# Optimization experiments

Measured on AMD Instinct MI355X. Metric: run time of the kernel, lower is better.

The kernel has to match this reference:

```python
import jax, jax.numpy as jnp
import numpy as np

B, L, D, H, HD, FF, NL = 2, 2048, 1024, 16, 64, 4096, 2
EPS = 1e-5
NEG = -1e30


def setup_inputs() -> dict:
    key = jax.random.key(0)
    ks = jax.random.split(key, 20)
    x = jax.random.normal(ks[0], (B, L, D), jnp.float32)
    # RoPE tables, rotate-half convention: [L, HD]
    pos = jnp.arange(L, dtype=jnp.float32)
    freqs = 1.0 / (10000.0 ** (jnp.arange(0, HD, 2, dtype=jnp.float32) / HD))
    ang = pos[:, None] * freqs[None, :]              # [L, HD/2]
    cos = jnp.concatenate([jnp.cos(ang), jnp.cos(ang)], -1)
    sin = jnp.concatenate([jnp.sin(ang), jnp.sin(ang)], -1)
    s = 0.02
    wq = jax.random.normal(ks[1], (NL, D, D), jnp.float32) * s
    wk = jax.random.normal(ks[2], (NL, D, D), jnp.float32) * s
    wv = jax.random.normal(ks[3], (NL, D, D), jnp.float32) * s
    wo = jax.random.normal(ks[4], (NL, D, D), jnp.float32) * s
    w1 = jax.random.normal(ks[5], (NL, D, FF), jnp.float32) * s
    w2 = jax.random.normal(ks[6], (NL, FF, D), jnp.float32) * s
    w3 = jax.random.normal(ks[7], (NL, D, FF), jnp.float32) * s
    attn_norm = jnp.ones((NL, D), jnp.float32)
    mlp_norm = jnp.ones((NL, D), jnp.float32)
    final_norm = jnp.ones((D,), jnp.float32)
    rw1 = jax.random.normal(ks[8], (D, D), jnp.float32) * s
    rb1 = jnp.zeros((D,), jnp.float32)
    rw2 = jax.random.normal(ks[9], (D, 1), jnp.float32) * s
    rb2 = jnp.zeros((1,), jnp.float32)
    return dict(x=x, cos=cos, sin=sin, wq=wq, wk=wk, wv=wv, wo=wo,
                w1=w1, w2=w2, w3=w3, attn_norm=attn_norm, mlp_norm=mlp_norm,
                final_norm=final_norm, rw1=rw1, rb1=rb1, rw2=rw2, rb2=rb2)


def _rms(x, w):
    return x * jax.lax.rsqrt(jnp.mean(x * x, -1, keepdims=True) + EPS) * w


def _rope(t, cos, sin):
    # t: [B, L, H, HD]; cos/sin: [L, HD]
    t1, t2 = jnp.split(t, 2, axis=-1)
    rot = jnp.concatenate([-t2, t1], -1)
    return t * cos[None, :, None, :] + rot * sin[None, :, None, :]


def reference(x, cos, sin, wq, wk, wv, wo, w1, w2, w3,
              attn_norm, mlp_norm, final_norm, rw1, rb1, rw2, rb2):
    causal = jnp.tril(jnp.ones((L, L), bool))
    h = x
    for i in range(NL):  # small fixed layer loop
        a = _rms(h, attn_norm[i])
        q = _rope((a @ wq[i]).reshape(B, L, H, HD), cos, sin)
        k = _rope((a @ wk[i]).reshape(B, L, H, HD), cos, sin)
        v = (a @ wv[i]).reshape(B, L, H, HD)
        sc = jnp.einsum('bqhd,bkhd->bhqk', q, k) / np.float32(np.sqrt(HD))
        sc = jnp.where(causal, sc, NEG)
        o = jnp.einsum('bhqk,bkhd->bqhd', jax.nn.softmax(sc, -1), v)
        h = h + o.reshape(B, L, D) @ wo[i]
        m = _rms(h, mlp_norm[i])
        h = h + (jax.nn.silu(m @ w1[i]) * (m @ w3[i])) @ w2[i]
    h = _rms(h, final_norm)

    # router chunking: straight-through hard boundaries
    logits = (jax.nn.silu(h @ rw1 + rb1) @ rw2 + rb2)[..., 0]   # [B, L]
    probs = jax.nn.sigmoid(logits)
    hard = (probs > 0.5).astype(h.dtype)
    mask = probs + jax.lax.stop_gradient(hard - probs)
    mask = mask.at[:, 0].set(1.0)
    mhard = jax.lax.stop_gradient(mask)
    # select matrix: S padded to static upper bound L (rows >= counts are zero)
    cums = jnp.cumsum(mhard, -1)                                # [B, L]
    seg = jnp.arange(1, L + 1, dtype=cums.dtype)[None, :, None] # [1, S, 1]
    assignment = (cums[:, None, :] == seg).astype(h.dtype)      # [B, S, L]
    select = assignment * mask[:, None, :]
    compressed = jnp.einsum('bsl,bld->bsd', select, h)          # [B, S, D]
    boundary_positions = jnp.argsort(-mhard, axis=-1)           # stable in jax
    counts = mhard.sum(-1).astype(jnp.int32)
    avg_chunk_size = jnp.float32(L) / jnp.mean(counts.astype(jnp.float32))
    return (h, compressed, boundary_positions, counts, avg_chunk_size)
```

## Files before the change

### kernel.cpp

```cpp
#include <hip/hip_runtime.h>
#include <cmath>

#define B_  2
#define L_  2048
#define D_  1024
#define H_  16
#define FF_ 4096
#define NL_ 2
#define NT_ (B_*L_)
#define ND_ (NT_*D_)

typedef __attribute__((ext_vector_type(8))) short bf16x8;
typedef __attribute__((ext_vector_type(4))) float f32x4;

__device__ __forceinline__ short f2bf(float x){
  unsigned u = __builtin_bit_cast(unsigned, x);
  unsigned r = (u + 0x7fffu + ((u>>16)&1u)) >> 16;
  return (short)r;
}
__device__ __forceinline__ float bf2f(short s){
  unsigned u = ((unsigned)(unsigned short)s) << 16;
  return __builtin_bit_cast(float, u);
}
#define MFMA16(a,b,c) __builtin_amdgcn_mfma_f32_16x16x32_bf16(a,b,c,0,0,0)

__device__ __forceinline__ void gload16(const short* g, short* l){
  __builtin_amdgcn_global_load_lds((const __attribute__((address_space(1))) void*)g,
                                   (__attribute__((address_space(3))) void*)l, 16, 0, 0);
}

__device__ __forceinline__ int2 xcd_swizzle(){
  int gx = gridDim.x;
  int n  = gx * gridDim.y;
  int hw = blockIdx.x + gx*blockIdx.y;
  int logical = (hw&7)*(n>>3) + (hw>>3);
  return make_int2(logical % gx, logical / gx);
}

template<bool WF32>
__global__ __launch_bounds__(256) void k_rmsnorm_s(const float* __restrict__ in,
                                                   const float* __restrict__ w,
                                                   short* __restrict__ oh,
                                                   short* __restrict__ ol,
                                                   float* __restrict__ of){
  int row = blockIdx.x; int tid = threadIdx.x;
  float4 xv = ((const float4*)(in + (size_t)row*D_))[tid];
  float ss = xv.x*xv.x + xv.y*xv.y + xv.z*xv.z + xv.w*xv.w;
  #pragma unroll
  for (int off=32; off; off>>=1) ss += __shfl_xor(ss, off);
  __shared__ float wsum[4];
  if ((tid&63)==0) wsum[tid>>6] = ss;
  __syncthreads();
  float tot = wsum[0]+wsum[1]+wsum[2]+wsum[3];
  float scale = 1.0f / sqrtf(tot*(1.0f/(float)D_) + 1e-5f);
  float4 w4 = ((const float4*)w)[tid];
  float v[4] = {xv.x*scale*w4.x, xv.y*scale*w4.y, xv.z*scale*w4.z, xv.w*scale*w4.w};
  short4 hh, ll;
  short h0=f2bf(v[0]); hh.x=h0; ll.x=f2bf(v[0]-bf2f(h0));
  short h1=f2bf(v[1]); hh.y=h1; ll.y=f2bf(v[1]-bf2f(h1));
  short h2=f2bf(v[2]); hh.z=h2; ll.z=f2bf(v[2]-bf2f(h2));
  short h3=f2bf(v[3]); hh.w=h3; ll.w=f2bf(v[3]-bf2f(h3));
  *(short4*)(oh + (size_t)row*D_ + tid*4) = hh;
  *(short4*)(ol + (size_t)row*D_ + tid*4) = ll;
  if (WF32){
    float4 ov; ov.x=v[0]; ov.y=v[1]; ov.z=v[2]; ov.w=v[3];
    ((float4*)(of + (size_t)row*D_))[tid] = ov;
  }
}

__device__ __forceinline__ void wsplit_body(float (*t)[68], const float* __restrict__ src,
                                            short* __restrict__ dh, short* __restrict__ dl,
                                            int srcN, int kOff, int nOff, int KT,
                                            int bx, int by){
  int k0 = bx*64, n0v = by*64;
  int tid = threadIdx.x;
  #pragma unroll
  for (int p=0;p<4;p++){
    int r = p*16 + (tid>>4);
    int c4 = (tid&15)*4;
    float4 v = *(const float4*)(src + (size_t)(kOff + k0 + r)*srcN + nOff + n0v + c4);
    *(float4*)&t[r][c4] = v;
  }
  __syncthreads();
  int n = tid>>2, kk = (tid&3)*16;
  bf16x8 H0, L0, H1, L1;
  #pragma unroll
  for (int q=0;q<8;q++){
    float v = t[kk+q][n]; short h=f2bf(v); H0[q]=h; L0[q]=f2bf(v-bf2f(h));
  }
  #pragma unroll
  for (int q=0;q<8;q++){
    float v = t[kk+8+q][n]; short h=f2bf(v); H1[q]=h; L1[q]=f2bf(v-bf2f(h));
  }
  size_t dof = (size_t)(n0v + n)*KT + k0 + kk;
  *(bf16x8*)(dh + dof) = H0;  *(bf16x8*)(dh + dof + 8) = H1;
  *(bf16x8*)(dl + dof) = L0;  *(bf16x8*)(dl + dof + 8) = L1;
}

__global__ __launch_bounds__(256) void k_wsplit(const float* __restrict__ src,
                                                short* __restrict__ dh,
                                                short* __restrict__ dl,
                                                int srcN, int kOff, int nOff, int KT){
  __shared__ float t[64][68];
  wsplit_body(t, src, dh, dl, srcN, kOff, nOff, KT, blockIdx.x, blockIdx.y);
}

__global__ __launch_bounds__(256) void k_wsplit_qkv(const float* __restrict__ wq,
                                                    const float* __restrict__ wk,
                                                    const float* __restrict__ wv,
                                                    short* __restrict__ dh,
                                                    short* __restrict__ dl){
  __shared__ float t[64][68];
  int z = blockIdx.z;
  const float* s = (z==0)?wq:(z==1)?wk:wv;
  wsplit_body(t, s, dh + (size_t)z*1048576, dl + (size_t)z*1048576,
              1024, 0, 0, 1024, blockIdx.x, blockIdx.y);
}

__global__ __launch_bounds__(256) void k_wsplit_ffn(const float* __restrict__ w1,
                                                    const float* __restrict__ w3,
                                                    const float* __restrict__ w2,
                                                    short* __restrict__ w1h, short* __restrict__ w1l,
                                                    short* __restrict__ w3h, short* __restrict__ w3l,
                                                    short* __restrict__ w2h, short* __restrict__ w2l,
                                                    int hc){
  __shared__ float t[64][68];
  int z = blockIdx.z;
  if (z < 2){
    if (blockIdx.x >= 16) return;
    const float* s = z ? w3 : w1;
    wsplit_body(t, s, z?w3h:w1h, z?w3l:w1l, 4096, 0, hc*2048, 1024, blockIdx.x, blockIdx.y);
  } else {
    if (blockIdx.y >= 16) return;
    wsplit_body(t, w2, w2h, w2l, 1024, hc*2048, 0, 2048, blockIdx.x, blockIdx.y);
  }
}

__global__ __launch_bounds__(256,3) void k_qkv_mm(const short* __restrict__ Ah,
                                                  const short* __restrict__ Al,
                                                  const short* __restrict__ Wh,
                                                  const short* __restrict__ Wl,
                                                  short* __restrict__ OutH,
                                                  short* __restrict__ Vf){
  __shared__ short lds[32768];
  int tid = threadIdx.x, wid = tid>>6, lane = tid&63;
  int l15 = lane&15, l4 = lane>>4;
  int wr = wid>>1, wc = wid&1;
  int2 bxy = xcd_swizzle();
  int m0 = bxy.y*128, n0 = bxy.x*128;
  const int K = 1024;
  f32x4 acc[4][4];
  #pragma unroll
  for (int i=0;i<4;i++){
    #pragma unroll
    for (int j=0;j<4;j++) acc[i][j] = (f32x4){0.f,0.f,0.f,0.f};
  }
  const short* gsrc = (wid==0)?Ah:(wid==1)?Al:(wid==2)?Wh:Wl;
  int rb = (wid<2)? m0 : n0;
  int gcol = ((lane&7)^(lane>>3))*8;
  short* ldsw = lds + wid*8192;
  const short* gp0 = gsrc + (size_t)(rb + (lane>>3))*K + gcol;
  for (int k0=0; k0<K; k0+=64){
    const short* gp = gp0 + k0;
    #pragma unroll
    for (int lc=0; lc<16; ++lc)
      gload16(gp + (size_t)lc*8*K, ldsw + lc*512);
    __syncthreads();
    #pragma unroll
    for (int ks=0; ks<2; ++ks){
      bf16x8 af[4], alf[4], wf[4], wlf[4];
      int gs = ((ks*4 + l4) ^ (lane&7))*8;
      #pragma unroll
      for (int f=0; f<4; ++f){
        int ar = (wr*64 + f*16 + l15)*64 + gs;
        af[f]  = *(const bf16x8*)&lds[ar];
        alf[f] = *(const bf16x8*)&lds[8192 + ar];
        int wr2 = (wc*64 + f*16 + l15)*64 + gs;
        wf[f]  = *(const bf16x8*)&lds[16384 + wr2];
        wlf[f] = *(const bf16x8*)&lds[24576 + wr2];
      }
      __builtin_amdgcn_s_setprio(1);
      #pragma unroll
      for (int i=0;i<4;i++){
        #pragma unroll
        for (int j=0;j<4;j++){
          acc[i][j] = MFMA16(af[i],  wf[j],  acc[i][j]);
          acc[i][j] = MFMA16(alf[i], wf[j],  acc[i][j]);
          acc[i][j] = MFMA16(af[i],  wlf[j], acc[i][j]);
        }
      }
      __builtin_amdgcn_s_setprio(0);
    }
    __syncthreads();
  }
  int sel = n0 >> 10;
  int cb = (n0 & 1023) + wc*64;
  if (sel < 2){
    short* oh = OutH + (size_t)sel*8388608;
    short* ol = oh + 4194304;
    #pragma unroll
    for (int i=0;i<4;i++){
      #pragma unroll
      for (int j=0;j<4;j++){
        #pragma unroll
        for (int r=0;r<4;r++){
          size_t mg = (size_t)(m0 + wr*64 + i*16 + l4*4 + r);
          int ng = cb + j*16 + l15;
          float v = acc[i][j][r];
          short h = f2bf(v);
          oh[mg*1024 + ng] = h;
          ol[mg*1024 + ng] = f2bf(v - bf2f(h));
        }
      }
    }
  } else {
    #pragma unroll
    for (int i=0;i<4;i++){
      #pragma unroll
      for (int j=0;j<4;j++){
        #pragma unroll
        for (int r=0;r<4;r++){
          int mg = m0 + wr*64 + i*16 + l4*4 + r;
          int ng = cb + j*16 + l15;
          float v = acc[i][j][r];
          short hh2 = f2bf(v);
          short ll2 = f2bf(v - bf2f(hh2));
          int bb = mg >> 11, tt = mg & 2047;
          int hd = ng >> 6, kc = tt >> 5;
          int l4v = (tt>>3)&3, iv = tt&7;
          int dtv = (ng>>4)&3, l15v = ng&15;
          size_t base = ((size_t)((bb*16+hd)*64 + kc)*8 + dtv*2)*512 + (l4v*16+l15v)*8 + iv;
          Vf[base] = hh2;
          Vf[base + 512] = ll2;
        }
      }
    }
  }
}

template<int EPI>
__global__ __launch_bounds__(256,(EPI==3)?3:4) void k_mm64(const short* __restrict__ Ah,
                                                const short* __restrict__ Al,
                                                const short* __restrict__ Wh,
                                                const short* __restrict__ Wl,
                                                const short* __restrict__ W3h,
                                                const short* __restrict__ W3l,
                                                int K,
                                                float* __restrict__ Cf,
                                                const float* __restrict__ bias,
                                                short* __restrict__ Gh,
                                                short* __restrict__ Gl,
                                                int ldc){
  __shared__ short lds[(EPI==3)?32768:24576];
  int tid = threadIdx.x, wid = tid>>6, lane = tid&63;
  int l15 = lane&15, l4 = lane>>4;
  int2 bxy = xcd_swizzle();
  int m0 = bxy.y*128, n0 = bxy.x*64;
  f32x4 a1[2][4], a3[2][4];
  #pragma unroll
  for (int i=0;i<2;i++){
    #pragma unroll
    for (int j=0;j<4;j++){ a1[i][j]=(f32x4){0.f,0.f,0.f,0.f}; a3[i][j]=(f32x4){0.f,0.f,0.f,0.f}; }
  }
  int gcol = ((lane&7)^(lane>>3))*8;
  int l8 = lane>>3;
  const int NCH = (EPI==3)? 16 : 12;
  for (int k0=0; k0<K; k0+=64){
    for (int t=0; t<NCH; ++t){
      int c = wid*NCH + t;
      const short* sb; int row0; short* db;
      if (c < 32){
        sb = (c<16)? Ah : Al; row0 = m0 + (c&15)*8;
        db = lds + ((c<16)?0:8192) + (c&15)*512;
      } else {
        int wseg = (c-32)>>3;
        sb = (wseg==0)?Wh:(wseg==1)?Wl:(wseg==2)?W3h:W3l;
        row0 = n0 + (c&7)*8;
        db = lds + 16384 + wseg*4096 + (c&7)*512;
      }
      gload16(sb + (size_t)(row0 + l8)*K + k0 + gcol, db);
    }
    __syncthreads();
    #pragma unroll
    for (int ks=0; ks<2; ++ks){
      int gs = ((ks*4 + l4) ^ (lane&7))*8;
      bf16x8 af[2], alf[2], wh[4], wl[4];
      #pragma unroll
      for (int f=0; f<2; ++f){
        int ar = (wid*32 + f*16 + l15)*64 + gs;
        af[f]  = *(const bf16x8*)&lds[ar];
        alf[f] = *(const bf16x8*)&lds[8192 + ar];
      }
      #pragma unroll
      for (int f=0; f<4; ++f){
        int wr2 = (f*16 + l15)*64 + gs;
        wh[f] = *(const bf16x8*)&lds[16384 + wr2];
        wl[f] = *(const bf16x8*)&lds[20480 + wr2];
      }
      __builtin_amdgcn_s_setprio(1);
      #pragma unroll
      for (int i=0;i<2;i++){
        #pragma unroll
        for (int j=0;j<4;j++){
          a1[i][j] = MFMA16(af[i],  wh[j], a1[i][j]);
          a1[i][j] = MFMA16(alf[i], wh[j], a1[i][j]);
          a1[i][j] = MFMA16(af[i],  wl[j], a1[i][j]);
        }
      }
      __builtin_amdgcn_s_setprio(0);
      if (EPI==3){
        bf16x8 w3h[4], w3l[4];
        #pragma unroll
        for (int f=0; f<4; ++f){
          int wr2 = (f*16 + l15)*64 + gs;
          w3h[f] = *(const bf16x8*)&lds[24576 + wr2];
          w3l[f] = *(const bf16x8*)&lds[28672 + wr2];
        }
        __builtin_amdgcn_s_setprio(1);
        #pragma unroll
        for (int i=0;i<2;i++){
          #pragma unroll
          for (int j=0;j<4;j++){
            a3[i][j] = MFMA16(af[i],  w3h[j], a3[i][j]);
            a3[i][j] = MFMA16(alf[i], w3h[j], a3[i][j]);
            a3[i][j] = MFMA16(af[i],  w3l[j], a3[i][j]);
          }
        }
        __builtin_amdgcn_s_setprio(0);
      }
    }
    __syncthreads();
  }
  #pragma unroll
  for (int i=0;i<2;i++){
    #pragma unroll
    for (int j=0;j<4;j++){
      #pragma unroll
      for (int r=0;r<4;r++){
        size_t mg = (size_t)(m0 + wid*32 + i*16 + l4*4 + r);
        int ng = n0 + j*16 + l15;
        float v = a1[i][j][r];
        if (EPI==1){
          float* cp = Cf + mg*ldc + ng;
          *cp = *cp + v;
        } else if (EPI==2){
          float x = v + bias[ng];
          Cf[mg*ldc + ng] = x/(1.f+expf(-x));
        } else {
          float g = v/(1.f+expf(-v)) * a3[i][j][r];
          short h = f2bf(g);
          Gh[mg*2048 + ng] = h;
          Gl[mg*2048 + ng] = f2bf(g - bf2f(h));
        }
      }
    }
  }
}

__global__ __launch_bounds__(256) void k_prep_k_wo(const short* __restrict__ kh,
                                                   const short* __restrict__ kl,
                                                   const float* __restrict__ cosT,
                                                   const float* __restrict__ sinT,
                                                   short* __restrict__ kf,
                                                   const float* __restrict__ wo,
                                                   short* __restrict__ woh,
                                                   short* __restrict__ wol){
  __shared__ float t[64][68];
  int x = blockIdx.x;
  if (x >= 1024){
    int idx = x - 1024;
    wsplit_body(t, wo, woh, wol, 1024, 0, 0, 1024, idx & 15, idx >> 4);
    return;
  }
  int wave = threadIdx.x>>6, lane = threadIdx.x&63;
  int t16 = (x & 31)*4 + wave;
  int bh = x >> 5; int b = bh>>4, h = bh&15;
  int l15 = lane&15, l4 = lane>>4;
  int tok = t16*16 + l15;
  const short* khp = kh + (size_t)(b*L_+tok)*D_ + h*64;
  const short* klp = kl + (size_t)(b*L_+tok)*D_ + h*64;
  int d0 = l4*8;
  bf16x8 ka  = *(const bf16x8*)(khp + d0);
  bf16x8 kb2 = *(const bf16x8*)(khp + 32 + d0);
  bf16x8 kla = *(const bf16x8*)(klp + d0);
  bf16x8 klb = *(const bf16x8*)(klp + 32 + d0);
  const float* cr = cosT + (size_t)tok*64;
  const float* sr = sinT + (size_t)tok*64;
  float c0[8], s0[8], c1[8], s1[8];
  *(float4*)&c0[0] = *(const float4*)(cr + d0);      *(float4*)&c0[4] = *(const float4*)(cr + d0 + 4);
  *(float4*)&c1[0] = *(const float4*)(cr + 32 + d0); *(float4*)&c1[4] = *(const float4*)(cr + 32 + d0 + 4);
  *(float4*)&s0[0] = *(const float4*)(sr + d0);      *(float4*)&s0[4] = *(const float4*)(sr + d0 + 4);
  *(float4*)&s1[0] = *(const float4*)(sr + 32 + d0); *(float4*)&s1[4] = *(const float4*)(sr + 32 + d0 + 4);
  bf16x8 h0, lo0, h1, lo1;
  #pragma unroll
  for (int j=0;j<8;j++){
    float k0v = bf2f(ka[j]) + bf2f(kla[j]);
    float k1v = bf2f(kb2[j]) + bf2f(klb[j]);
    float r0 = k0v*c0[j] - k1v*s0[j];
    float r1 = k1v*c1[j] + k0v*s1[j];
    short a = f2bf(r0); h0[j]=a; lo0[j]=f2bf(r0 - bf2f(a));
    short bS = f2bf(r1); h1[j]=bS; lo1[j]=f2bf(r1 - bf2f(bS));
  }
  size_t base = ((size_t)(bh*128 + t16)*4)*512 + lane*8;
  *(bf16x8*)(kf + base)        = h0;
  *(bf16x8*)(kf + base + 512)  = lo0;
  *(bf16x8*)(kf + base + 1024) = h1;
  *(bf16x8*)(kf + base + 1536) = lo1;
}

__global__ __launch_bounds__(256) void k_attn_mfma(const short* __restrict__ qhb,
                                                   const short* __restrict__ qlb,
                                                   const short* __restrict__ kf,
                                                   const short* __restrict__ vf,
                                                   const float* __restrict__ cosT,
                                                   const float* __restrict__ sinT,
                                                   short* __restrict__ oh,
                                                   short* __restrict__ ol){
  int bid = blockIdx.x;
  int logical = (bid&7)*64 + (bid>>3);
  int bh = logical>>4, pair = logical&15;
  int b = bh>>4, h = bh&15;
  int wave = threadIdx.x>>6, lane = threadIdx.x&63;
  int l15 = lane&15, l4 = lane>>4;
  __shared__ short kvs[2][16384];
  __shared__ short pblob[4][2048];
  short* pb = pblob[wave];

  auto stage = [&](int bufi, int kt){
    const short* kg = kf + ((size_t)(bh*128 + kt*4))*2048;
    const short* vg = vf + ((size_t)(bh*64 + kt*2))*4096;
    short* dst = kvs[bufi];
    #pragma unroll
    for (int c=0;c<8;c++){
      int ch = wave*8 + c;
      const short* src = (ch<16)? (kg + ch*512) : (vg + (ch-16)*512);
      gload16(src + lane*8, dst + ch*512);
    }
  };

  for (int half=0; half<2; ++half){
    int qt = (half==0) ? (31-pair) : pair;
    stage(0, 0);
    int tok = qt*64 + wave*16 + l15;
    const short* qhp = qhb + (size_t)(b*L_+tok)*D_ + h*64;
    const short* qlp = qlb + (size_t)(b*L_+tok)*D_ + h*64;
    int d0 = l4*8;
    bf16x8 qa  = *(const bf16x8*)(qhp + d0);
    bf16x8 qb2 = *(const bf16x8*)(qhp + 32 + d0);
    bf16x8 qla = *(const bf16x8*)(qlp + d0);
    bf16x8 qlb2= *(const bf16x8*)(qlp + 32 + d0);
    const float* cr = cosT + (size_t)tok*64;
    const float* sr = sinT + (size_t)tok*64;
    float c0[8], s0[8], c1[8], s1[8];
    *(float4*)&c0[0] = *(const float4*)(cr + d0);      *(float4*)&c0[4] = *(const float4*)(cr + d0 + 4);
    *(float4*)&c1[0] = *(const float4*)(cr + 32 + d0); *(float4*)&c1[4] = *(const float4*)(cr + 32 + d0 + 4);
    *(float4*)&s0[0] = *(const float4*)(sr + d0);      *(float4*)&s0[4] = *(const float4*)(sr + d0 + 4);
    *(float4*)&s1[0] = *(const float4*)(sr + 32 + d0); *(float4*)&s1[4] = *(const float4*)(sr + 32 + d0 + 4);
    bf16x8 qh0, ql0, qh1, ql1;
    #pragma unroll
    for (int j=0;j<8;j++){
      float q0v = bf2f(qa[j]) + bf2f(qla[j]);
      float q1v = bf2f(qb2[j]) + bf2f(qlb2[j]);
      float r0 = (q0v*c0[j] - q1v*s0[j]) * 0.125f;
      float r1 = (q1v*c1[j] + q0v*s1[j]) * 0.125f;
      short a = f2bf(r0); qh0[j]=a; ql0[j]=f2bf(r0 - bf2f(a));
      short bS = f2bf(r1); qh1[j]=bS; ql1[j]=f2bf(r1 - bf2f(bS));
    }

    f32x4 O[4];
    #pragma unroll
    for (int dt=0;dt<4;dt++) O[dt] = (f32x4){0.f,0.f,0.f,0.f};
    float m_[4] = {-1e30f,-1e30f,-1e30f,-1e30f};
    float ls[4] = {0.f,0.f,0.f,0.f};

    int cur = 0;
    for (int kt=0; kt<=qt; ++kt){
      bool haveNext = (kt < qt);
      if (haveNext){
        stage(cur^1, kt+1);
        asm volatile("s_waitcnt vmcnt(8)" ::: "memory");
      } else {
        asm volatile("s_waitcnt vmcnt(0)" ::: "memory");
      }
      __builtin_amdgcn_s_barrier();
      const short* Kl = kvs[cur];
      const short* Vl = kvs[cur] + 8192;
      bool dtile = (kt == qt);
      f32x4 sr4[4];
      #pragma unroll
      for (int g=0; g<4; g++){
        f32x4 acc = (f32x4){0.f,0.f,0.f,0.f};
        if (!(dtile && g > wave)){
          const short* kp = Kl + g*2048 + lane*8;
          bf16x8 kh0 = *(const bf16x8*)(kp);
          bf16x8 kl0 = *(const bf16x8*)(kp + 512);
          bf16x8 kh1 = *(const bf16x8*)(kp + 1024);
          bf16x8 kl1 = *(const bf16x8*)(kp + 1536);
          __builtin_amdgcn_s_setprio(1);
          acc = MFMA16(qh0, kh0, acc); acc = MFMA16(qh1, kh1, acc);
          acc = MFMA16(ql0, kh0, acc); acc = MFMA16(ql1, kh1, acc);
          acc = MFMA16(qh0, kl0, acc); acc = MFMA16(qh1, kl1, acc);
          __builtin_amdgcn_s_setprio(0);
        }
        sr4[g] = acc;
      }
      float p_[4][4];
      #pragma unroll
      for (int r=0; r<4; r++){
        int rowrel = wave*16 + l4*4 + r;
        float mx = -1e30f;
        float sv[4];
        #pragma unroll
        for (int g=0; g<4; g++){
          float v = sr4[g][r];
          if (dtile && (g*16 + l15) > rowrel) v = -1e30f;
          sv[g] = v; mx = fmaxf(mx, v);
        }
        #pragma unroll
        for (int off=1; off<16; off<<=1) mx = fmaxf(mx, __shfl_xor(mx, off));
        float nm = fmaxf(m_[r], mx);
        float al = __expf(m_[r] - nm);
        m_[r] = nm;
        float ps = 0.f;
        #pragma unroll
        for (int g=0; g<4; g++){ float pv = __expf(sv[g] - nm); p_[g][r] = pv; ps += pv; }
        #pragma unroll
        for (int off=1; off<16; off<<=1) ps += __shfl_xor(ps, off);
        ls[r] = ls[r]*al + ps;
        #pragma unroll
        for (int dt=0; dt<4; dt++) O[dt][r] *= al;
      }
      #pragma unroll
      for (int g=0; g<4; g++){
        int key = g*16 + l15;
        int cc = key>>5, sub = (key>>3)&3, ii = key&7;
        #pragma unroll
        for (int r=0; r<4; r++){
          float pv = p_[g][r];
          short ph = f2bf(pv);
          short pl = f2bf(pv - bf2f(ph));
          int idx = cc*1024 + (sub*16 + l4*4 + r)*8 + ii;
          pb[idx] = ph;
          pb[idx + 512] = pl;
        }
      }
      asm volatile("s_waitcnt lgkmcnt(0)" ::: "memory");
      #pragma unroll
      for (int cc=0; cc<2; cc++){
        bf16x8 pah = *(const bf16x8*)(pb + cc*1024 + lane*8);
        bf16x8 pal = *(const bf16x8*)(pb + cc*1024 + 512 + lane*8);
        const short* vp = Vl + cc*4096 + lane*8;
        __builtin_amdgcn_s_setprio(1);
        #pragma unroll
        for (int dt=0; dt<4; dt++){
          bf16x8 vh = *(const bf16x8*)(vp + dt*1024);
          bf16x8 vl = *(const bf16x8*)(vp + dt*1024 + 512);
          O[dt] = MFMA16(pah, vh, O[dt]);
          O[dt] = MFMA16(pal, vh, O[dt]);
          O[dt] = MFMA16(pah, vl, O[dt]);
        }
        __builtin_amdgcn_s_setprio(0);
      }
      __builtin_amdgcn_s_barrier();
      cur ^= 1;
    }
    #pragma unroll
    for (int r=0; r<4; r++){
      float inv = 1.0f / ls[r];
      size_t row = (size_t)(b*L_ + qt*64 + wave*16 + l4*4 + r);
      #pragma unroll
      for (int dt=0; dt<4; dt++){
        float v = O[dt][r]*inv;
        short hh = f2bf(v);
        oh[row*D_ + h*64 + dt*16 + l15] = hh;
        ol[row*D_ + h*64 + dt*16 + l15] = f2bf(v - bf2f(hh));
      }
    }
  }
}

__global__ __launch_bounds__(256) void k_gemv(const float* __restrict__ T,
                                              const float* __restrict__ rw2,
                                              const float* __restrict__ rb2,
                                              float* __restrict__ logits){
  int row = blockIdx.x; int tid = threadIdx.x;
  float4 tv = ((const float4*)(T + (size_t)row*D_))[tid];
  float4 wv = ((const float4*)rw2)[tid];
  float s = tv.x*wv.x + tv.y*wv.y + tv.z*wv.z + tv.w*wv.w;
  #pragma unroll
  for (int off=32; off; off>>=1) s += __shfl_xor(s, off);
  __shared__ float ps[4];
  if ((tid&63)==0) ps[tid>>6] = s;
  __syncthreads();
  if (tid==0) logits[row] = ps[0]+ps[1]+ps[2]+ps[3] + rb2[0];
}

__global__ __launch_bounds__(256) void k_boundary(const float* __restrict__ logits,
                                                  float* __restrict__ pos_out,
                                                  int* __restrict__ hard,
                                                  int* __restrict__ cums,
                                                  int* __restrict__ counts){
  int b = blockIdx.x; int tid = threadIdx.x;
  __shared__ int part[256];
  int loc[8]; int s=0;
  int base = b*L_;
  #pragma unroll
  for (int j=0;j<8;j++){
    int ll = tid*8 + j;
    float lg = logits[base+ll];
    int hv = (ll==0) ? 1 : ((lg > 0.0f) ? 1 : 0);
    loc[j]=hv; s+=hv;
  }
  part[tid]=s; __syncthreads();
  for (int off=1; off<256; off<<=1){
    int v = part[tid];
    int add = (tid>=off) ? part[tid-off] : 0;
    __syncthreads();
    part[tid] = v + add;
    __syncthreads();
  }
  int total = part[255];
  int run = part[tid] - s;
  #pragma unroll
  for (int j=0;j<8;j++){
    int ll = tid*8+j;
    run += loc[j];
    hard[base+ll] = loc[j];
    cums[base+ll] = run;
    int idx = loc[j] ? (run-1) : (total + ll - run);
    pos_out[base+idx] = (float)ll;
  }
  if (tid==0) counts[b] = total;
}

__global__ __launch_bounds__(256) void k_scatter(const float* __restrict__ hf,
                                                 const int* __restrict__ hard,
                                                 const int* __restrict__ cums,
                                                 float* __restrict__ comp){
  int rowid = blockIdx.x;
  if (!hard[rowid]) return;
  int b = rowid >> 11;
  int s = cums[rowid]-1;
  const float4* src = (const float4*)(hf + (size_t)rowid*D_);
  float4* dst = (float4*)(comp + (size_t)(b*L_ + s)*D_);
  dst[threadIdx.x] = src[threadIdx.x];
}

__global__ void k_finalize(const int* __restrict__ counts, float* __restrict__ out){
  if (threadIdx.x==0 && blockIdx.x==0){
    float c0 = (float)counts[0], c1 = (float)counts[1];
    out[0]=c0; out[1]=c1;
    out[2] = (float)L_ / (0.5f*(c0+c1));
  }
}

extern "C" void kernel_launch(void* const* d_in, const int* in_sizes, int n_in,
                              void* d_out, int out_size, void* d_ws, size_t ws_size,
                              hipStream_t stream){
  const float* x      = (const float*)d_in[0];
  const float* cosT   = (const float*)d_in[1];
  const float* sinT   = (const float*)d_in[2];
  const float* wq     = (const float*)d_in[3];
  const float* wk     = (const float*)d_in[4];
  const float* wv     = (const float*)d_in[5];
  const float* wo     = (const float*)d_in[6];
  const float* w1     = (const float*)d_in[7];
  const float* w2     = (const float*)d_in[8];
  const float* w3     = (const float*)d_in[9];
  const float* attn_n = (const float*)d_in[10];
  const float* mlp_n  = (const float*)d_in[11];
  const float* final_n= (const float*)d_in[12];
  const float* rw1    = (const float*)d_in[13];
  const float* rb1    = (const float*)d_in[14];
  const float* rw2    = (const float*)d_in[15];
  const float* rb2    = (const float*)d_in[16];

  float* outF = (float*)d_out;
  float* hD   = outF;
  float* compD= outF + (size_t)ND_;
  float* posD = outF + (size_t)2*ND_;

  char* WS = (char*)d_ws;
  auto S = [&](size_t mb){ return (short*)(WS + mb*1048576ull); };
  auto F = [&](size_t mb){ return (float*)(WS + mb*1048576ull); };
  short *ah=S(0), *al=S(8);
  short *qh=S(16), *ql=S(24), *kh=S(32), *kl=S(40);
  short *qkvwt_h=S(48), *qkvwt_l=S(54);
  short *vf=S(64);
  short *kf=S(48);
  short *wot_h=S(0), *wot_l=S(2);
  short *gh=S(16), *gl=S(32);
  short *w1t_h=S(48), *w1t_l=S(52), *w3t_h=S(56), *w3t_l=S(60);
  short *w2t_h=S(64), *w2t_l=S(68);
  short *rw1t_h=S(16), *rw1t_l=S(18);
  float *ra=F(20);
  float *logits=F(76);
  int *hard=(int*)(logits+NT_), *cums=hard+NT_, *cnts=cums+NT_;
  short *oh=(short*)compD, *ol=oh+4194304;

  hipMemcpyAsync(hD, x, (size_t)ND_*sizeof(float), hipMemcpyDeviceToDevice, stream);

  for (int i=0;i<NL_;++i){
    k_rmsnorm_s<false><<<NT_,256,0,stream>>>(hD, attn_n + (size_t)i*D_, ah, al, nullptr);
    k_wsplit_qkv<<<dim3(16,16,3),256,0,stream>>>(wq + (size_t)i*D_*D_, wk + (size_t)i*D_*D_,
                                                 wv + (size_t)i*D_*D_, qkvwt_h, qkvwt_l);
    k_qkv_mm<<<dim3(24,32),256,0,stream>>>(ah, al, qkvwt_h, qkvwt_l, qh, vf);
    k_prep_k_wo<<<dim3(1280),256,0,stream>>>(kh, kl, cosT, sinT, kf,
                                             wo + (size_t)i*D_*D_, wot_h, wot_l);
    k_attn_mfma<<<dim3(512),256,0,stream>>>(qh, ql, kf, vf, cosT, sinT, oh, ol);
    k_mm64<1><<<dim3(16,32),256,0,stream>>>(oh, ol, wot_h, wot_l, nullptr, nullptr,
                                            1024, hD, nullptr, nullptr, nullptr, 1024);
    k_rmsnorm_s<false><<<NT_,256,0,stream>>>(hD, mlp_n + (size_t)i*D_, ah, al, nullptr);
    for (int hc=0; hc<2; ++hc){
      k_wsplit_ffn<<<dim3(32,32,3),256,0,stream>>>(w1 + (size_t)i*D_*FF_, w3 + (size_t)i*D_*FF_,
                                                   w2 + (size_t)i*FF_*D_,
                                                   w1t_h, w1t_l, w3t_h, w3t_l, w2t_h, w2t_l, hc);
      k_mm64<3><<<dim3(32,32),256,0,stream>>>(ah, al, w1t_h, w1t_l, w3t_h, w3t_l,
                                              1024, nullptr, nullptr, gh, gl, 0);
      k_mm64<1><<<dim3(16,32),256,0,stream>>>(gh, gl, w2t_h, w2t_l, nullptr, nullptr,
                                              2048, hD, nullptr, nullptr, nullptr, 1024);
    }
  }
  k_rmsnorm_s<true><<<NT_,256,0,stream>>>(hD, final_n, ah, al, hD);
  k_wsplit<<<dim3(16,16),256,0,stream>>>(rw1, rw1t_h, rw1t_l, 1024, 0, 0, 1024);
  k_mm64<2><<<dim3(16,32),256,0,stream>>>(ah, al, rw1t_h, rw1t_l, nullptr, nullptr,
                                          1024, ra, rb1, nullptr, nullptr, 1024);
  k_gemv<<<NT_,256,0,stream>>>(ra, rw2, rb2, logits);
  k_boundary<<<B_,256,0,stream>>>(logits, posD, hard, cums, cnts);
  hipMemsetAsync(compD, 0, (size_t)ND_*sizeof(float), stream);
  k_scatter<<<NT_,256,0,stream>>>(hD, hard, cums, compD);
  k_finalize<<<1,64,0,stream>>>(cnts, posD + NT_);
}
```

Measured before the change: 1.250 ms.

## Replace 128x64 GEMM with 128x128 tiles and interleave w1/w3 columns

The GEMM kernel goes from a 128x64 tile to a 128x128 tile on a 2x2 wave grid, with each wave loading one operand plane into LDS. The separate w3 path is removed: w1 and w3 columns are interleaved into one weight matrix, so the gated FFN becomes a single GEMM whose epilogue pairs neighbouring lanes with a shuffle to form silu(a)*b. The aim is more arithmetic per byte loaded and simpler load code. In exchange, occupancy drops to 2 blocks, the output-projection GEMMs launch half as many blocks, and half the lanes sit idle in the gate epilogue.

```diff
diff --git a/kernel.cpp b/kernel.cpp
--- a/kernel.cpp
+++ b/kernel.cpp
@@ -71,7 +71,7 @@
 __device__ __forceinline__ void wsplit_body(float (*t)[68], const float* __restrict__ src,
                                             short* __restrict__ dh, short* __restrict__ dl,
                                             int srcN, int kOff, int nOff, int KT,
-                                            int bx, int by){
+                                            int bx, int by, int colStride, int colOff){
   int k0 = bx*64, n0v = by*64;
   int tid = threadIdx.x;
   #pragma unroll
@@ -92,7 +92,7 @@
   for (int q=0;q<8;q++){
     float v = t[kk+8+q][n]; short h=f2bf(v); H1[q]=h; L1[q]=f2bf(v-bf2f(h));
   }
-  size_t dof = (size_t)(n0v + n)*KT + k0 + kk;
+  size_t dof = (size_t)(colOff + colStride*(n0v + n))*KT + k0 + kk;
   *(bf16x8*)(dh + dof) = H0;  *(bf16x8*)(dh + dof + 8) = H1;
   *(bf16x8*)(dl + dof) = L0;  *(bf16x8*)(dl + dof + 8) = L1;
 }
@@ -102,7 +102,7 @@
                                                 short* __restrict__ dl,
                                                 int srcN, int kOff, int nOff, int KT){
   __shared__ float t[64][68];
-  wsplit_body(t, src, dh, dl, srcN, kOff, nOff, KT, blockIdx.x, blockIdx.y);
+  wsplit_body(t, src, dh, dl, srcN, kOff, nOff, KT, blockIdx.x, blockIdx.y, 1, 0);
 }
 
 __global__ __launch_bounds__(256) void k_wsplit_qkv(const float* __restrict__ wq,
@@ -114,14 +114,13 @@
   int z = blockIdx.z;
   const float* s = (z==0)?wq:(z==1)?wk:wv;
   wsplit_body(t, s, dh + (size_t)z*1048576, dl + (size_t)z*1048576,
-              1024, 0, 0, 1024, blockIdx.x, blockIdx.y);
+              1024, 0, 0, 1024, blockIdx.x, blockIdx.y, 1, 0);
 }
 
 __global__ __launch_bounds__(256) void k_wsplit_ffn(const float* __restrict__ w1,
                                                     const float* __restrict__ w3,
                                                     const float* __restrict__ w2,
-                                                    short* __restrict__ w1h, short* __restrict__ w1l,
-                                                    short* __restrict__ w3h, short* __restrict__ w3l,
+                                                    short* __restrict__ w13h, short* __restrict__ w13l,
                                                     short* __restrict__ w2h, short* __restrict__ w2l,
                                                     int hc){
   __shared__ float t[64][68];
@@ -129,10 +128,10 @@
   if (z < 2){
     if (blockIdx.x >= 16) return;
     const float* s = z ? w3 : w1;
-    wsplit_body(t, s, z?w3h:w1h, z?w3l:w1l, 4096, 0, hc*2048, 1024, blockIdx.x, blockIdx.y);
+    wsplit_body(t, s, w13h, w13l, 4096, 0, hc*2048, 1024, blockIdx.x, blockIdx.y, 2, z);
   } else {
     if (blockIdx.y >= 16) return;
-    wsplit_body(t, w2, w2h, w2l, 1024, hc*2048, 0, 2048, blockIdx.x, blockIdx.y);
+    wsplit_body(t, w2, w2h, w2l, 1024, hc*2048, 0, 2048, blockIdx.x, blockIdx.y, 1, 0);
   }
 }
 
@@ -239,107 +238,75 @@
 }
 
 template<int EPI>
-__global__ __launch_bounds__(256,(EPI==3)?3:4) void k_mm64(const short* __restrict__ Ah,
-                                                const short* __restrict__ Al,
-                                                const short* __restrict__ Wh,
-                                                const short* __restrict__ Wl,
-                                                const short* __restrict__ W3h,
-                                                const short* __restrict__ W3l,
-                                                int K,
-                                                float* __restrict__ Cf,
-                                                const float* __restrict__ bias,
-                                                short* __restrict__ Gh,
-                                                short* __restrict__ Gl,
-                                                int ldc){
-  __shared__ short lds[(EPI==3)?32768:24576];
+__global__ __launch_bounds__(256,2) void k_mm128(const short* __restrict__ Ah,
+                                                 const short* __restrict__ Al,
+                                                 const short* __restrict__ Wh,
+                                                 const short* __restrict__ Wl,
+                                                 int K,
+                                                 float* __restrict__ Cf,
+                                                 const float* __restrict__ bias,
+                                                 short* __restrict__ Gh,
+                                                 short* __restrict__ Gl,
+                                                 int ldc){
+  __shared__ short lds[32768];
   int tid = threadIdx.x, wid = tid>>6, lane = tid&63;
   int l15 = lane&15, l4 = lane>>4;
+  int wr = wid>>1, wc = wid&1;
   int2 bxy = xcd_swizzle();
-  int m0 = bxy.y*128, n0 = bxy.x*64;
-  f32x4 a1[2][4], a3[2][4];
-  #pragma unroll
-  for (int i=0;i<2;i++){
-    #pragma unroll
-    for (int j=0;j<4;j++){ a1[i][j]=(f32x4){0.f,0.f,0.f,0.f}; a3[i][j]=(f32x4){0.f,0.f,0.f,0.f}; }
-  }
+  int m0 = bxy.y*128, n0 = bxy.x*128;
+  f32x4 acc[4][4];
+  #pragma unroll
+  for (int i=0;i<4;i++){
+    #pragma unroll
+    for (int j=0;j<4;j++) acc[i][j] = (f32x4){0.f,0.f,0.f,0.f};
+  }
+  const short* gsrc = (wid==0)?Ah:(wid==1)?Al:(wid==2)?Wh:Wl;
+  int rb = (wid<2)? m0 : n0;
   int gcol = ((lane&7)^(lane>>3))*8;
-  int l8 = lane>>3;
-  const int NCH = (EPI==3)? 16 : 12;
+  short* ldsw = lds + wid*8192;
+  const short* gp0 = gsrc + (size_t)(rb + (lane>>3))*K + gcol;
   for (int k0=0; k0<K; k0+=64){
-    for (int t=0; t<NCH; ++t){
-      int c = wid*NCH + t;
-      const short* sb; int row0; short* db;
-      if (c < 32){
-        sb = (c<16)? Ah : Al; row0 = m0 + (c&15)*8;
-        db = lds + ((c<16)?0:8192) + (c&15)*512;
-      } else {
-        int wseg = (c-32)>>3;
-        sb = (wseg==0)?Wh:(wseg==1)?Wl:(wseg==2)?W3h:W3l;
-        row0 = n0 + (c&7)*8;
-        db = lds + 16384 + wseg*4096 + (c&7)*512;
-      }
-      gload16(sb + (size_t)(row0 + l8)*K + k0 + gcol, db);
-    }
+    const short* gp = gp0 + k0;
+    #pragma unroll
+    for (int lc=0; lc<16; ++lc)
+      gload16(gp + (size_t)lc*8*K, ldsw + lc*512);
     __syncthreads();
     #pragma unroll
     for (int ks=0; ks<2; ++ks){
+      bf16x8 af[4], alf[4], wf[4], wlf[4];
       int gs = ((ks*4 + l4) ^ (lane&7))*8;
-      bf16x8 af[2], alf[2], wh[4], wl[4];
-      #pragma unroll
-      for (int f=0; f<2; ++f){
-        int ar = (wid*32 + f*16 + l15)*64 + gs;
+      #pragma unroll
+      for (int f=0; f<4; ++f){
+        int ar = (wr*64 + f*16 + l15)*64 + gs;
         af[f]  = *(const bf16x8*)&lds[ar];
         alf[f] = *(const bf16x8*)&lds[8192 + ar];
-      }
-      #pragma unroll
-      for (int f=0; f<4; ++f){
-        int wr2 = (f*16 + l15)*64 + gs;
-        wh[f] = *(const bf16x8*)&lds[16384 + wr2];
-        wl[f] = *(const bf16x8*)&lds[20480 + wr2];
+        int wr2 = (wc*64 + f*16 + l15)*64 + gs;
+        wf[f]  = *(const bf16x8*)&lds[16384 + wr2];
+        wlf[f] = *(const bf16x8*)&lds[24576 + wr2];
       }
       __builtin_amdgcn_s_setprio(1);
       #pragma unroll
-      for (int i=0;i<2;i++){
+      for (int i=0;i<4;i++){
         #pragma unroll
         for (int j=0;j<4;j++){
-          a1[i][j] = MFMA16(af[i],  wh[j], a1[i][j]);
-          a1[i][j] = MFMA16(alf[i], wh[j], a1[i][j]);
-          a1[i][j] = MFMA16(af[i],  wl[j], a1[i][j]);
+          acc[i][j] = MFMA16(af[i],  wf[j],  acc[i][j]);
+          acc[i][j] = MFMA16(alf[i], wf[j],  acc[i][j]);
+          acc[i][j] = MFMA16(af[i],  wlf[j], acc[i][j]);
         }
       }
       __builtin_amdgcn_s_setprio(0);
-      if (EPI==3){
-        bf16x8 w3h[4], w3l[4];
-        #pragma unroll
-        for (int f=0; f<4; ++f){
-          int wr2 = (f*16 + l15)*64 + gs;
-          w3h[f] = *(const bf16x8*)&lds[24576 + wr2];
-          w3l[f] = *(const bf16x8*)&lds[28672 + wr2];
-        }
-        __builtin_amdgcn_s_setprio(1);
-        #pragma unroll
-        for (int i=0;i<2;i++){
-          #pragma unroll
-          for (int j=0;j<4;j++){
-            a3[i][j] = MFMA16(af[i],  w3h[j], a3[i][j]);
-            a3[i][j] = MFMA16(alf[i], w3h[j], a3[i][j]);
-            a3[i][j] = MFMA16(af[i],  w3l[j], a3[i][j]);
-          }
-        }
-        __builtin_amdgcn_s_setprio(0);
-      }
     }
     __syncthreads();
   }
   #pragma unroll
-  for (int i=0;i<2;i++){
+  for (int i=0;i<4;i++){
     #pragma unroll
     for (int j=0;j<4;j++){
       #pragma unroll
       for (int r=0;r<4;r++){
-        size_t mg = (size_t)(m0 + wid*32 + i*16 + l4*4 + r);
-        int ng = n0 + j*16 + l15;
-        float v = a1[i][j][r];
+        size_t mg = (size_t)(m0 + wr*64 + i*16 + l4*4 + r);
+        int ng = n0 + wc*64 + j*16 + l15;
+        float v = acc[i][j][r];
         if (EPI==1){
           float* cp = Cf + mg*ldc + ng;
           *cp = *cp + v;
@@ -347,10 +314,14 @@
           float x = v + bias[ng];
           Cf[mg*ldc + ng] = x/(1.f+expf(-x));
         } else {
-          float g = v/(1.f+expf(-v)) * a3[i][j][r];
-          short h = f2bf(g);
-          Gh[mg*2048 + ng] = h;
-          Gl[mg*2048 + ng] = f2bf(g - bf2f(h));
+          float a3v = __shfl_xor(v, 1);
+          if ((lane & 1) == 0){
+            float g = v/(1.f+expf(-v)) * a3v;
+            short h = f2bf(g);
+            size_t go = mg*ldc + (ng>>1);
+            Gh[go] = h;
+            Gl[go] = f2bf(g - bf2f(h));
+          }
         }
       }
     }
@@ -369,7 +340,7 @@
   int x = blockIdx.x;
   if (x >= 1024){
     int idx = x - 1024;
-    wsplit_body(t, wo, woh, wol, 1024, 0, 0, 1024, idx & 15, idx >> 4);
+    wsplit_body(t, wo, woh, wol, 1024, 0, 0, 1024, idx & 15, idx >> 4, 1, 0);
     return;
   }
   int wave = threadIdx.x>>6, lane = threadIdx.x&63;
@@ -690,7 +661,7 @@
   short *kf=S(48);
   short *wot_h=S(0), *wot_l=S(2);
   short *gh=S(16), *gl=S(32);
-  short *w1t_h=S(48), *w1t_l=S(52), *w3t_h=S(56), *w3t_l=S(60);
+  short *w13t_h=S(48), *w13t_l=S(56);
   short *w2t_h=S(64), *w2t_l=S(68);
   short *rw1t_h=S(16), *rw1t_l=S(18);
   float *ra=F(20);
@@ -708,22 +679,22 @@
     k_prep_k_wo<<<dim3(1280),256,0,stream>>>(kh, kl, cosT, sinT, kf,
                                              wo + (size_t)i*D_*D_, wot_h, wot_l);
     k_attn_mfma<<<dim3(512),256,0,stream>>>(qh, ql, kf, vf, cosT, sinT, oh, ol);
-    k_mm64<1><<<dim3(16,32),256,0,stream>>>(oh, ol, wot_h, wot_l, nullptr, nullptr,
+    k_mm128<1><<<dim3(8,32),256,0,stream>>>(oh, ol, wot_h, wot_l,
                                             1024, hD, nullptr, nullptr, nullptr, 1024);
     k_rmsnorm_s<false><<<NT_,256,0,stream>>>(hD, mlp_n + (size_t)i*D_, ah, al, nullptr);
     for (int hc=0; hc<2; ++hc){
       k_wsplit_ffn<<<dim3(32,32,3),256,0,stream>>>(w1 + (size_t)i*D_*FF_, w3 + (size_t)i*D_*FF_,
                                                    w2 + (size_t)i*FF_*D_,
-                                                   w1t_h, w1t_l, w3t_h, w3t_l, w2t_h, w2t_l, hc);
-      k_mm64<3><<<dim3(32,32),256,0,stream>>>(ah, al, w1t_h, w1t_l, w3t_h, w3t_l,
-                                              1024, nullptr, nullptr, gh, gl, 0);
-      k_mm64<1><<<dim3(16,32),256,0,stream>>>(gh, gl, w2t_h, w2t_l, nullptr, nullptr,
+                                                   w13t_h, w13t_l, w2t_h, w2t_l, hc);
+      k_mm128<3><<<dim3(32,32),256,0,stream>>>(ah, al, w13t_h, w13t_l,
+                                               1024, nullptr, nullptr, gh, gl, 2048);
+      k_mm128<1><<<dim3(8,32),256,0,stream>>>(gh, gl, w2t_h, w2t_l,
                                               2048, hD, nullptr, nullptr, nullptr, 1024);
     }
   }
   k_rmsnorm_s<true><<<NT_,256,0,stream>>>(hD, final_n, ah, al, hD);
   k_wsplit<<<dim3(16,16),256,0,stream>>>(rw1, rw1t_h, rw1t_l, 1024, 0, 0, 1024);
-  k_mm64<2><<<dim3(16,32),256,0,stream>>>(ah, al, rw1t_h, rw1t_l, nullptr, nullptr,
+  k_mm128<2><<<dim3(8,32),256,0,stream>>>(ah, al, rw1t_h, rw1t_l,
                                           1024, ra, rb1, nullptr, nullptr, 1024);
   k_gemv<<<NT_,256,0,stream>>>(ra, rw2, rb2, logits);
   k_boundary<<<B_,256,0,stream>>>(logits, posD, hard, cums, cnts);
```

Result: slower. 1.350 ms (+8.0%).
